# Optimization experiments

Hardware: AMD Instinct MI355X
Metric: run time of the kernel (lower is better)

Reference implementation:

```python
import jax, jax.numpy as jnp
import numpy as np

EMBED, HEADS, LEVELS, POINTS = 256, 8, 4, 4
SPATIAL_SHAPES = np.array([[128, 128], [64, 64], [32, 32], [16, 16]], dtype=np.int32)


def _grid_init_bias():
    # Faithful reproduction of the sampling_offsets bias init (per-head directional grid).
    thetas = np.arange(HEADS, dtype=np.float32) * (2.0 * np.pi / HEADS)
    g = np.stack([np.cos(thetas), np.sin(thetas)], -1)
    g = g / np.abs(g).max(-1, keepdims=True)
    g = np.tile(g.reshape(HEADS, 1, 1, 2), (1, LEVELS, POINTS, 1))
    for i in range(POINTS):
        g[:, :, i, :] *= i + 1
    return g.reshape(-1).astype(np.float32)


def setup_inputs() -> dict:
    key = jax.random.key(0)
    ks = jax.random.split(key, 8)
    bs = 2
    V = int((SPATIAL_SHAPES[:, 0] * SPATIAL_SHAPES[:, 1]).sum())  # 21760
    Q = V  # encoder self-attention
    C = EMBED
    n_off = HEADS * LEVELS * POINTS * 2
    n_attn = HEADS * LEVELS * POINTS
    inv_sqrt_c = 1.0 / np.sqrt(C)
    return {
        "query": jax.random.normal(ks[0], (bs, Q, C), jnp.float32),
        "value": jax.random.normal(ks[1], (bs, V, C), jnp.float32),
        "reference_points": jax.random.uniform(ks[2], (bs, Q, LEVELS, 2), jnp.float32),
        "spatial_shapes": SPATIAL_SHAPES,  # static int array
        # learned parameters (torch Linear stored as [in, out]: y = x @ W + b)
        "W_off": jax.random.normal(ks[3], (C, n_off), jnp.float32) * 0.01,
        "b_off": jnp.asarray(_grid_init_bias()),
        "W_attn": jax.random.normal(ks[4], (C, n_attn), jnp.float32) * 0.02,
        "b_attn": jnp.zeros((n_attn,), jnp.float32),
        "W_v": jax.random.normal(ks[5], (C, C), jnp.float32) * inv_sqrt_c,
        "b_v": jnp.zeros((C,), jnp.float32),
        "W_out": jax.random.normal(ks[6], (C, C), jnp.float32) * inv_sqrt_c,
        "b_out": jnp.zeros((C,), jnp.float32),
    }


def _ms_deform_attn(query, value, reference_points, shapes,
                    W_off, b_off, W_attn, b_attn, W_v, b_v, W_out, b_out):
    bs, Q, C = query.shape
    d = C // HEADS
    # value projection -> [bs, heads, V, d]
    val = (value @ W_v + b_v).reshape(bs, -1, HEADS, d).transpose(0, 2, 1, 3)
    # sampling offsets and attention weights from query
    off = (query @ W_off + b_off).reshape(bs, Q, HEADS, LEVELS, POINTS, 2)
    attn = jax.nn.softmax(
        (query @ W_attn + b_attn).reshape(bs, Q, HEADS, LEVELS * POINTS), axis=-1
    ).reshape(bs, Q, HEADS, LEVELS, POINTS)
    # offset normalizer is (W, H) per level
    norm = jnp.asarray(np.stack([shapes[:, 1], shapes[:, 0]], -1), jnp.float32)  # [L,2]
    loc = reference_points[:, :, None, :, None, :] + off / norm[None, None, None, :, None, :]

    out = jnp.zeros((bs, HEADS, Q, d), query.dtype)
    start = 0
    for l in range(LEVELS):
        H, W = int(shapes[l, 0]), int(shapes[l, 1])
        v_l = val[:, :, start:start + H * W]  # [bs, heads, H*W, d]
        start += H * W
        loc_l = loc[:, :, :, l]    # [bs, Q, heads, P, 2] in [0,1]
        attn_l = attn[:, :, :, l]  # [bs, Q, heads, P]
        # grid_sample(align_corners=False, padding_mode='zeros') semantics
        g = 2.0 * loc_l - 1.0
        x = (g[..., 0] + 1.0) * 0.5 * W - 0.5
        y = (g[..., 1] + 1.0) * 0.5 * H - 0.5
        x0 = jnp.floor(x)
        y0 = jnp.floor(y)
        for dx in (0, 1):
            for dy in (0, 1):
                xi = x0 + dx
                yi = y0 + dy
                w = (1.0 - jnp.abs(x - xi)) * (1.0 - jnp.abs(y - yi))
                valid = (xi >= 0) & (xi <= W - 1) & (yi >= 0) & (yi <= H - 1)
                w = jnp.where(valid, w, 0.0) * attn_l  # fused corner + attention weight
                idx = (jnp.clip(yi, 0, H - 1).astype(jnp.int32) * W
                       + jnp.clip(xi, 0, W - 1).astype(jnp.int32))  # [bs,Q,heads,P]
                idx_t = jnp.transpose(idx, (0, 2, 1, 3)).reshape(bs, HEADS, Q * POINTS)
                vals = jnp.take_along_axis(v_l, idx_t[..., None], axis=2)
                vals = vals.reshape(bs, HEADS, Q, POINTS, d)
                out = out + jnp.einsum('bhqpd,bqhp->bhqd', vals, w)
    out = out.transpose(0, 2, 1, 3).reshape(bs, Q, C)  # heads-major channel layout
    return out @ W_out + b_out


def reference(query, value, reference_points, spatial_shapes,
              W_off, b_off, W_attn, b_attn, W_v, b_v, W_out, b_out):
    shapes = np.asarray(spatial_shapes)  # static
    return _ms_deform_attn(query, value, reference_points, shapes,
                           W_off, b_off, W_attn, b_attn, W_v, b_v, W_out, b_out)
```

## Files before the change

kernel.cpp:

```cpp
#include <hip/hip_runtime.h>
#include <math.h>

#define QN 21760
#define MTOT 43520
#define SZBQC 11141120

typedef __attribute__((ext_vector_type(8))) short bf16x8;
typedef __attribute__((ext_vector_type(4))) float f32x4;

__device__ inline ushort f2bf(float f) {
  union { float f; uint u; } v; v.f = f;
  return (ushort)((v.u + 0x7FFFu + ((v.u >> 16) & 1u)) >> 16);
}
__device__ inline uint pk2(float lo, float hi) { return (uint)f2bf(lo) | ((uint)f2bf(hi) << 16); }

__device__ inline void g2l(const ushort* g, ushort* l) {
  __builtin_amdgcn_global_load_lds(
      (const __attribute__((address_space(1))) void*)g,
      (__attribute__((address_space(3))) void*)l, 16, 0, 0);
}

__global__ __launch_bounds__(256) void prep_weights(
    const float* __restrict__ Wv, const float* __restrict__ Wout,
    const float* __restrict__ Woff, const float* __restrict__ Wattn,
    const float* __restrict__ boff, const float* __restrict__ battn,
    ushort* __restrict__ wv_t, ushort* __restrict__ wout_t,
    ushort* __restrict__ wol_t, float* __restrict__ biasf) {
  int bidx = blockIdx.x, t = threadIdx.x;
  if (bidx < 256) {
    int idx = bidx * 256 + t; int n = idx >> 8, k = idx & 255;
    wv_t[idx] = f2bf(Wv[(size_t)k * 256 + n]);
  } else if (bidx < 512) {
    int idx = (bidx - 256) * 256 + t; int n = idx >> 8, k = idx & 255;
    wout_t[idx] = f2bf(Wout[(size_t)k * 256 + n]);
  } else {
    int idx = (bidx - 512) * 256 + t; int n = idx >> 8, k = idx & 255;
    float v = (n < 256) ? Woff[(size_t)k * 256 + n] : Wattn[(size_t)k * 128 + (n - 256)];
    wol_t[idx] = f2bf(v);
    if (idx < 384) biasf[idx] = (idx < 256) ? boff[idx] : battn[idx - 256];
  }
}


__global__ __launch_bounds__(256) void gemm_in(
    const float* __restrict__ value, const float* __restrict__ query,
    const ushort* __restrict__ Wv, const ushort* __restrict__ Wol,
    const float* __restrict__ bv, const float* __restrict__ bol,
    ushort* __restrict__ val_out, float* __restrict__ offlog) {
  __shared__ ushort As[2][4096];
  __shared__ ushort Bs[2][4096];
  const int bid = blockIdx.x;
  const int q5  = bid >> 3;
  const int bxv = (bid & 7) + 8 * (q5 / 5);
  const int bx  = q5 % 5;
  if (bxv >= 340) return;
  const int t = threadIdx.x, wave = t >> 6, lane = t & 63;
  const int bm = bxv * 128;
  const bool isVal = bx < 2;
  const float* A   = isVal ? value : query;
  const ushort* Bt = isVal ? (Wv + (size_t)bx * 128 * 256)
                           : (Wol + (size_t)(bx - 2) * 128 * 256);
  const int wm = (wave >> 1) * 64, wn = (wave & 1) * 64;
  const int l15 = lane & 15, l4 = lane >> 4;
  const int pc = l4 ^ ((l15 >> 1) & 3);

  const int srow = lane >> 2;
  const int sch  = (lane & 3) ^ ((lane >> 3) & 3);
  const ushort* Bg = Bt + (size_t)(32 * wave + srow) * 256 + sch * 8;
  ushort* lb[2] = { &Bs[0][(32 * wave) * 32], &Bs[1][(32 * wave) * 32] };

  f32x4 acc[4][4];
#pragma unroll
  for (int i = 0; i < 4; ++i)
#pragma unroll
    for (int j = 0; j < 4; ++j) acc[i][j] = (f32x4){0.f, 0.f, 0.f, 0.f};

  int arow[4], apart[4];
#pragma unroll
  for (int i = 0; i < 4; ++i) {
    int c = t + i * 256; arow[i] = c >> 3; apart[i] = c & 7;
  }

  {
    float4 pa[4];
#pragma unroll
    for (int i = 0; i < 4; ++i)
      pa[i] = *(const float4*)&A[(size_t)(bm + arow[i]) * 256 + apart[i] * 4];
    g2l(Bg, lb[0]); g2l(Bg + 16 * 256, lb[0] + 16 * 32);
#pragma unroll
    for (int i = 0; i < 4; ++i) {
      int pc16 = (apart[i] >> 1) ^ ((arow[i] >> 1) & 3);
      ushort4 hv = { f2bf(pa[i].x), f2bf(pa[i].y), f2bf(pa[i].z), f2bf(pa[i].w) };
      *(ushort4*)&As[0][arow[i] * 32 + pc16 * 8 + (apart[i] & 1) * 4] = hv;
    }
  }

  for (int k = 0; k < 8; ++k) {
    __syncthreads();
    const int cur = k & 1, nxt = cur ^ 1;
    float4 pa[4];
    if (k < 7) {
      int k1 = (k + 1) * 32;
#pragma unroll
      for (int i = 0; i < 4; ++i)
        pa[i] = *(const float4*)&A[(size_t)(bm + arow[i]) * 256 + k1 + apart[i] * 4];
      g2l(Bg + k1, lb[nxt]); g2l(Bg + 16 * 256 + k1, lb[nxt] + 16 * 32);
    }
    bf16x8 af[4], bfr[4];
#pragma unroll
    for (int mi = 0; mi < 4; ++mi)
      af[mi] = *(const bf16x8*)&As[cur][(wm + mi * 16 + l15) * 32 + pc * 8];
#pragma unroll
    for (int ni = 0; ni < 4; ++ni)
      bfr[ni] = *(const bf16x8*)&Bs[cur][(wn + ni * 16 + l15) * 32 + pc * 8];
#pragma unroll
    for (int mi = 0; mi < 4; ++mi)
#pragma unroll
      for (int ni = 0; ni < 4; ++ni)
        acc[mi][ni] = __builtin_amdgcn_mfma_f32_16x16x32_bf16(af[mi], bfr[ni], acc[mi][ni], 0, 0, 0);
    if (k < 7) {
#pragma unroll
      for (int i = 0; i < 4; ++i) {
        int pc16 = (apart[i] >> 1) ^ ((arow[i] >> 1) & 3);
        ushort4 hv = { f2bf(pa[i].x), f2bf(pa[i].y), f2bf(pa[i].z), f2bf(pa[i].w) };
        *(ushort4*)&As[nxt][arow[i] * 32 + pc16 * 8 + (apart[i] & 1) * 4] = hv;
      }
    }
  }

  if (isVal) {
    _Float16* vo = (_Float16*)val_out;
#pragma unroll
    for (int mi = 0; mi < 4; ++mi)
#pragma unroll
      for (int ni = 0; ni < 4; ++ni) {
        int col = bx * 128 + wn + ni * 16 + l15;
        float bb = bv[col];
        int hh = col >> 5, c = col & 31;
#pragma unroll
        for (int r = 0; r < 4; ++r) {
          int row = bm + wm + mi * 16 + l4 * 4 + r;
          int b = (row >= QN) ? 1 : 0;
          int vpos = row - b * QN;
          vo[((size_t)(b * 8 + hh) * QN + vpos) * 32 + c] = (_Float16)(acc[mi][ni][r] + bb);
        }
      }
  } else {
#pragma unroll
    for (int mi = 0; mi < 4; ++mi)
#pragma unroll
      for (int ni = 0; ni < 4; ++ni) {
        int col = (bx - 2) * 128 + wn + ni * 16 + l15;
        float bb = bol[col];
#pragma unroll
        for (int r = 0; r < 4; ++r) {
          int row = bm + wm + mi * 16 + l4 * 4 + r;
          offlog[(size_t)row * 384 + col] = acc[mi][ni][r] + bb;
        }
      }
  }
}

__global__ __launch_bounds__(256) void gemm_out(
    const ushort* __restrict__ A, const ushort* __restrict__ Bt,
    const float* __restrict__ bias, float* __restrict__ C) {
  __shared__ ushort As[2][4096];
  __shared__ ushort Bs[2][4096];
  const int bid = blockIdx.x;
  const int q2  = bid >> 3;
  const int bxv = (bid & 7) + 8 * (q2 >> 1);
  const int byv = q2 & 1;
  if (bxv >= 340) return;
  const int t = threadIdx.x, wave = t >> 6, lane = t & 63;
  const int bm = bxv * 128, bn = byv * 128;
  const int wm = (wave >> 1) * 64, wn = (wave & 1) * 64;
  const int l15 = lane & 15, l4 = lane >> 4;
  const int pc = l4 ^ ((l15 >> 1) & 3);

  const int srow = lane >> 2;
  const int sch  = (lane & 3) ^ ((lane >> 3) & 3);
  const ushort* Ag = A + (size_t)(bm + 32 * wave + srow) * 256 + sch * 8;
  const ushort* Bg = Bt + (size_t)(bn + 32 * wave + srow) * 256 + sch * 8;
  ushort* la[2] = { &As[0][(32 * wave) * 32], &As[1][(32 * wave) * 32] };
  ushort* lb[2] = { &Bs[0][(32 * wave) * 32], &Bs[1][(32 * wave) * 32] };

  f32x4 acc[4][4];
#pragma unroll
  for (int i = 0; i < 4; ++i)
#pragma unroll
    for (int j = 0; j < 4; ++j) acc[i][j] = (f32x4){0.f, 0.f, 0.f, 0.f};

  g2l(Ag, la[0]); g2l(Ag + 16 * 256, la[0] + 16 * 32);
  g2l(Bg, lb[0]); g2l(Bg + 16 * 256, lb[0] + 16 * 32);

  for (int k = 0; k < 8; ++k) {
    __syncthreads();
    const int cur = k & 1, nxt = cur ^ 1;
    if (k < 7) {
      int k1 = (k + 1) * 32;
      g2l(Ag + k1, la[nxt]); g2l(Ag + 16 * 256 + k1, la[nxt] + 16 * 32);
      g2l(Bg + k1, lb[nxt]); g2l(Bg + 16 * 256 + k1, lb[nxt] + 16 * 32);
    }
    bf16x8 af[4], bfr[4];
#pragma unroll
    for (int mi = 0; mi < 4; ++mi)
      af[mi] = *(const bf16x8*)&As[cur][(wm + mi * 16 + l15) * 32 + pc * 8];
#pragma unroll
    for (int ni = 0; ni < 4; ++ni)
      bfr[ni] = *(const bf16x8*)&Bs[cur][(wn + ni * 16 + l15) * 32 + pc * 8];
#pragma unroll
    for (int mi = 0; mi < 4; ++mi)
#pragma unroll
      for (int ni = 0; ni < 4; ++ni)
        acc[mi][ni] = __builtin_amdgcn_mfma_f32_16x16x32_bf16(af[mi], bfr[ni], acc[mi][ni], 0, 0, 0);
  }

#pragma unroll
  for (int mi = 0; mi < 4; ++mi)
#pragma unroll
    for (int ni = 0; ni < 4; ++ni) {
      int col = bn + wn + ni * 16 + l15;
      float bb = bias[col];
#pragma unroll
      for (int r = 0; r < 4; ++r) {
        int row = bm + wm + mi * 16 + l4 * 4 + r;
        C[(size_t)row * 256 + col] = acc[mi][ni][r] + bb;
      }
    }
}

__device__ inline void fmah(float* a, uint4 u, float wv) {
  union { uint4 u; _Float16 h[8]; } c; c.u = u;
#pragma unroll
  for (int i = 0; i < 8; ++i) a[i] = fmaf((float)c.h[i], wv, a[i]);
}

__global__ __launch_bounds__(256) void msda_sample(
    const ushort* __restrict__ val, const float* __restrict__ offlog,
    const float* __restrict__ ref, ushort* __restrict__ interm) {
  int h   = blockIdx.x & 7;
  int z   = blockIdx.x >> 3;
  int sub = threadIdx.x & 3;
  int bq  = z * 64 + (threadIdx.x >> 2);
  int b   = (bq >= QN) ? 1 : 0;
  const uint sub8 = (uint)(sub * 8);
  const ushort* vb = val + (size_t)((uint)(b * 8 + h) * (uint)QN) * 32u + sub8;

  const float* lgp = offlog + (size_t)bq * 384 + 256 + h * 16;
  float4 lg = *(const float4*)(lgp + sub * 4);
  float m = fmaxf(fmaxf(lg.x, lg.y), fmaxf(lg.z, lg.w));
  m = fmaxf(m, __shfl_xor(m, 1, 64));
  m = fmaxf(m, __shfl_xor(m, 2, 64));
  float e0 = __expf(lg.x - m), e1 = __expf(lg.y - m),
        e2 = __expf(lg.z - m), e3 = __expf(lg.w - m);
  float s = e0 + e1 + e2 + e3;
  s += __shfl_xor(s, 1, 64);
  s += __shfl_xor(s, 2, 64);
  float inv = __builtin_amdgcn_rcpf(s);
  float aw[4] = { e0 * inv, e1 * inv, e2 * inv, e3 * inv };

  const int  Wl  = 128 >> sub;
  const uint t16 = 65536u >> (sub + sub);
  const int  lst = (int)((65536u - t16) / 3u);
  const float fW = (float)Wl;
  const float* offp = offlog + (size_t)bq * 384 + h * 32;
  float4 o0 = *(const float4*)(offp + sub * 8);
  float4 o1 = *(const float4*)(offp + sub * 8 + 4);
  float2 rf = *(const float2*)(ref + (size_t)bq * 8 + sub * 2);
  const float xb = rf.x * fW - 0.5f;
  const float yb = rf.y * fW - 0.5f;
  float ox[4] = { o0.x, o0.z, o1.x, o1.z };
  float oy[4] = { o0.y, o0.w, o1.y, o1.w };

  uint  pA0[4], pA1[4], pDX[4];
  float pX0[4], pX1[4], pY0[4], pY1[4];
#pragma unroll
  for (int p = 0; p < 4; ++p) {
    float x = xb + ox[p], y = yb + oy[p];
    float x0f = floorf(x), y0f = floorf(y);
    float fx = x - x0f, fy = y - y0f;
    int x0 = (int)x0f, y0 = (int)y0f;
    float a = aw[p];
    pX0[p] = ((uint)x0       < (uint)Wl) ? (1.f - fx) : 0.f;
    pX1[p] = ((uint)(x0 + 1) < (uint)Wl) ? fx         : 0.f;
    pY0[p] = (((uint)y0       < (uint)Wl) ? (1.f - fy) : 0.f) * a;
    pY1[p] = (((uint)(y0 + 1) < (uint)Wl) ? fy         : 0.f) * a;
    int xc0 = min(max(x0, 0), Wl - 1);
    int xc1 = min(max(x0 + 1, 0), Wl - 1);
    int yc0 = min(max(y0, 0), Wl - 1);
    int yc1 = min(max(y0 + 1, 0), Wl - 1);
    pA0[p] = (uint)((lst + yc0 * Wl + xc0) * 32);
    pA1[p] = (uint)((lst + yc1 * Wl + xc0) * 32);
    pDX[p] = (uint)((xc1 - xc0) * 32);
  }

  float acc[8];
#pragma unroll
  for (int i = 0; i < 8; ++i) acc[i] = 0.f;

  const int lanebase = (threadIdx.x & 63) & 60;
#pragma unroll
  for (int l = 0; l < 4; ++l) {
    const int src = lanebase | l;
#pragma unroll
    for (int p = 0; p < 4; ++p) {
      uint  A0  = (uint)__shfl((int)pA0[p], src, 64);
      uint  A1  = (uint)__shfl((int)pA1[p], src, 64);
      uint  DX  = (uint)__shfl((int)pDX[p], src, 64);
      float wx0 = __shfl(pX0[p], src, 64);
      float wx1 = __shfl(pX1[p], src, 64);
      float wy0 = __shfl(pY0[p], src, 64);
      float wy1 = __shfl(pY1[p], src, 64);
      uint4 u00 = *(const uint4*)(vb + A0);
      uint4 u01 = *(const uint4*)(vb + A0 + DX);
      uint4 u10 = *(const uint4*)(vb + A1);
      uint4 u11 = *(const uint4*)(vb + A1 + DX);
      fmah(acc, u00, wx0 * wy0);
      fmah(acc, u01, wx1 * wy0);
      fmah(acc, u10, wx0 * wy1);
      fmah(acc, u11, wx1 * wy1);
    }
  }

  uint4 o;
  o.x = pk2(acc[0], acc[1]); o.y = pk2(acc[2], acc[3]);
  o.z = pk2(acc[4], acc[5]); o.w = pk2(acc[6], acc[7]);
  *(uint4*)(interm + (size_t)bq * 256 + h * 32 + sub * 8) = o;
}

extern "C" void kernel_launch(void* const* d_in, const int* in_sizes, int n_in,
                              void* d_out, int out_size, void* d_ws, size_t ws_size,
                              hipStream_t stream) {
  const float* query = (const float*)d_in[0];
  const float* value = (const float*)d_in[1];
  const float* ref   = (const float*)d_in[2];
  const float* W_off  = (const float*)d_in[4];
  const float* b_off  = (const float*)d_in[5];
  const float* W_attn = (const float*)d_in[6];
  const float* b_attn = (const float*)d_in[7];
  const float* W_v    = (const float*)d_in[8];
  const float* b_v    = (const float*)d_in[9];
  const float* W_out  = (const float*)d_in[10];
  const float* b_out  = (const float*)d_in[11];
  float* out = (float*)d_out;

  char* wsb = (char*)d_ws;
  ushort* ws_wv     = (ushort*)(wsb + 0);
  ushort* ws_wol    = (ushort*)(wsb + 131072);
  ushort* ws_wout   = (ushort*)(wsb + 327680);
  float*  ws_biasf  = (float*)(wsb + 458752);
  ushort* ws_val    = (ushort*)(wsb + 462848);
  ushort* ws_interm = (ushort*)(wsb + 22745088);
  float*  ws_offlog = (float*)(wsb + 45027328);
  size_t need = (size_t)45027328 + 66846720;
  if (ws_size < need) return;

  dim3 blk(256);
  prep_weights<<<dim3(896), blk, 0, stream>>>(W_v, W_out, W_off, W_attn, b_off, b_attn,
                                              ws_wv, ws_wout, ws_wol, ws_biasf);
  gemm_in<<<dim3(1720), blk, 0, stream>>>(value, query, ws_wv, ws_wol, b_v, ws_biasf,
                                          ws_val, ws_offlog);
  msda_sample<<<dim3(5440), blk, 0, stream>>>(ws_val, ws_offlog, ref, ws_interm);
  gemm_out<<<dim3(688), blk, 0, stream>>>(ws_interm, ws_wout, b_out, out);
}
```

Before: 277.3 us.

## Pre-cast GEMM inputs to bf16, software-pipeline sampling gathers, use 2D grids

A new path converts value and query to bf16 in a prep pass whenever the workspace is large enough. The input GEMM can then stream bf16 tiles straight into LDS with direct global-to-LDS loads, replacing the in-kernel fp32 cast. The sampling kernel double-buffers its shuffle broadcasts and corner gathers, so the loads for the next point are issued before the current one is accumulated. The swizzled 1D block mapping in the GEMMs is also replaced by plain 2D grids, which may cost L2 locality and adds an extra read and write pass over the inputs.

```diff
diff --git a/kernel.cpp b/kernel.cpp
--- a/kernel.cpp
+++ b/kernel.cpp
@@ -24,8 +24,10 @@
     const float* __restrict__ Wv, const float* __restrict__ Wout,
     const float* __restrict__ Woff, const float* __restrict__ Wattn,
     const float* __restrict__ boff, const float* __restrict__ battn,
+    const float* __restrict__ value, const float* __restrict__ query,
     ushort* __restrict__ wv_t, ushort* __restrict__ wout_t,
-    ushort* __restrict__ wol_t, float* __restrict__ biasf) {
+    ushort* __restrict__ wol_t, float* __restrict__ biasf,
+    ushort* __restrict__ abf) {
   int bidx = blockIdx.x, t = threadIdx.x;
   if (bidx < 256) {
     int idx = bidx * 256 + t; int n = idx >> 8, k = idx & 255;
@@ -33,29 +35,121 @@
   } else if (bidx < 512) {
     int idx = (bidx - 256) * 256 + t; int n = idx >> 8, k = idx & 255;
     wout_t[idx] = f2bf(Wout[(size_t)k * 256 + n]);
-  } else {
+  } else if (bidx < 896) {
     int idx = (bidx - 512) * 256 + t; int n = idx >> 8, k = idx & 255;
     float v = (n < 256) ? Woff[(size_t)k * 256 + n] : Wattn[(size_t)k * 128 + (n - 256)];
     wol_t[idx] = f2bf(v);
     if (idx < 384) biasf[idx] = (idx < 256) ? boff[idx] : battn[idx - 256];
-  }
-}
-
-
-__global__ __launch_bounds__(256) void gemm_in(
+  } else {
+    int idx = (bidx - 896) * 2048 + t * 8;
+    const float* s = (idx < SZBQC) ? (value + idx) : (query + (idx - SZBQC));
+    float4 a = *(const float4*)s;
+    float4 c = *(const float4*)(s + 4);
+    uint4 o;
+    o.x = pk2(a.x, a.y); o.y = pk2(a.z, a.w);
+    o.z = pk2(c.x, c.y); o.w = pk2(c.z, c.w);
+    *(uint4*)&abf[idx] = o;
+  }
+}
+
+
+__global__ __launch_bounds__(256) void gemm_in_g2l(
+    const ushort* __restrict__ abf,
+    const ushort* __restrict__ Wv, const ushort* __restrict__ Wol,
+    const float* __restrict__ bv, const float* __restrict__ bol,
+    ushort* __restrict__ val_out, float* __restrict__ offlog) {
+  __shared__ ushort As[2][4096];
+  __shared__ ushort Bs[2][4096];
+  const int t = threadIdx.x, wave = t >> 6, lane = t & 63;
+  const int bx = blockIdx.y, bm = blockIdx.x * 128;
+  const bool isVal = bx < 2;
+  const ushort* A  = abf + (isVal ? 0 : SZBQC);
+  const ushort* Bt = isVal ? (Wv + (size_t)bx * 128 * 256)
+                           : (Wol + (size_t)(bx - 2) * 128 * 256);
+  const int wm = (wave >> 1) * 64, wn = (wave & 1) * 64;
+  const int l15 = lane & 15, l4 = lane >> 4;
+  const int pc = l4 ^ ((l15 >> 1) & 3);
+
+  const int srow = lane >> 2;
+  const int sch  = (lane & 3) ^ ((lane >> 3) & 3);
+  const ushort* Ag = A + (size_t)(bm + 32 * wave + srow) * 256 + sch * 8;
+  const ushort* Bg = Bt + (size_t)(32 * wave + srow) * 256 + sch * 8;
+  ushort* la[2] = { &As[0][(32 * wave) * 32], &As[1][(32 * wave) * 32] };
+  ushort* lb[2] = { &Bs[0][(32 * wave) * 32], &Bs[1][(32 * wave) * 32] };
+
+  f32x4 acc[4][4];
+#pragma unroll
+  for (int i = 0; i < 4; ++i)
+#pragma unroll
+    for (int j = 0; j < 4; ++j) acc[i][j] = (f32x4){0.f, 0.f, 0.f, 0.f};
+
+  g2l(Ag, la[0]); g2l(Ag + 16 * 256, la[0] + 16 * 32);
+  g2l(Bg, lb[0]); g2l(Bg + 16 * 256, lb[0] + 16 * 32);
+
+  for (int k = 0; k < 8; ++k) {
+    __syncthreads();
+    const int cur = k & 1, nxt = cur ^ 1;
+    if (k < 7) {
+      int k1 = (k + 1) * 32;
+      g2l(Ag + k1, la[nxt]); g2l(Ag + 16 * 256 + k1, la[nxt] + 16 * 32);
+      g2l(Bg + k1, lb[nxt]); g2l(Bg + 16 * 256 + k1, lb[nxt] + 16 * 32);
+    }
+    bf16x8 af[4], bfr[4];
+#pragma unroll
+    for (int mi = 0; mi < 4; ++mi)
+      af[mi] = *(const bf16x8*)&As[cur][(wm + mi * 16 + l15) * 32 + pc * 8];
+#pragma unroll
+    for (int ni = 0; ni < 4; ++ni)
+      bfr[ni] = *(const bf16x8*)&Bs[cur][(wn + ni * 16 + l15) * 32 + pc * 8];
+#pragma unroll
+    for (int mi = 0; mi < 4; ++mi)
+#pragma unroll
+      for (int ni = 0; ni < 4; ++ni)
+        acc[mi][ni] = __builtin_amdgcn_mfma_f32_16x16x32_bf16(af[mi], bfr[ni], acc[mi][ni], 0, 0, 0);
+  }
+
+  if (isVal) {
+    _Float16* vo = (_Float16*)val_out;
+#pragma unroll
+    for (int mi = 0; mi < 4; ++mi)
+#pragma unroll
+      for (int ni = 0; ni < 4; ++ni) {
+        int col = bx * 128 + wn + ni * 16 + l15;
+        float bb = bv[col];
+        int hh = col >> 5, c = col & 31;
+#pragma unroll
+        for (int r = 0; r < 4; ++r) {
+          int row = bm + wm + mi * 16 + l4 * 4 + r;
+          int b = (row >= QN) ? 1 : 0;
+          int vpos = row - b * QN;
+          vo[((size_t)(b * 8 + hh) * QN + vpos) * 32 + c] = (_Float16)(acc[mi][ni][r] + bb);
+        }
+      }
+  } else {
+#pragma unroll
+    for (int mi = 0; mi < 4; ++mi)
+#pragma unroll
+      for (int ni = 0; ni < 4; ++ni) {
+        int col = (bx - 2) * 128 + wn + ni * 16 + l15;
+        float bb = bol[col];
+#pragma unroll
+        for (int r = 0; r < 4; ++r) {
+          int row = bm + wm + mi * 16 + l4 * 4 + r;
+          offlog[(size_t)row * 384 + col] = acc[mi][ni][r] + bb;
+        }
+      }
+  }
+}
+
+__global__ __launch_bounds__(256) void gemm_in_cast(
     const float* __restrict__ value, const float* __restrict__ query,
     const ushort* __restrict__ Wv, const ushort* __restrict__ Wol,
     const float* __restrict__ bv, const float* __restrict__ bol,
     ushort* __restrict__ val_out, float* __restrict__ offlog) {
   __shared__ ushort As[2][4096];
   __shared__ ushort Bs[2][4096];
-  const int bid = blockIdx.x;
-  const int q5  = bid >> 3;
-  const int bxv = (bid & 7) + 8 * (q5 / 5);
-  const int bx  = q5 % 5;
-  if (bxv >= 340) return;
   const int t = threadIdx.x, wave = t >> 6, lane = t & 63;
-  const int bm = bxv * 128;
+  const int bx = blockIdx.y, bm = blockIdx.x * 128;
   const bool isVal = bx < 2;
   const float* A   = isVal ? value : query;
   const ushort* Bt = isVal ? (Wv + (size_t)bx * 128 * 256)
@@ -166,13 +260,8 @@
     const float* __restrict__ bias, float* __restrict__ C) {
   __shared__ ushort As[2][4096];
   __shared__ ushort Bs[2][4096];
-  const int bid = blockIdx.x;
-  const int q2  = bid >> 3;
-  const int bxv = (bid & 7) + 8 * (q2 >> 1);
-  const int byv = q2 & 1;
-  if (bxv >= 340) return;
   const int t = threadIdx.x, wave = t >> 6, lane = t & 63;
-  const int bm = bxv * 128, bn = byv * 128;
+  const int bm = blockIdx.x * 128, bn = blockIdx.y * 128;
   const int wm = (wave >> 1) * 64, wn = (wave & 1) * 64;
   const int l15 = lane & 15, l4 = lane >> 4;
   const int pc = l4 ^ ((l15 >> 1) & 3);
@@ -299,28 +388,42 @@
   for (int i = 0; i < 8; ++i) acc[i] = 0.f;
 
   const int lanebase = (threadIdx.x & 63) & 60;
-#pragma unroll
-  for (int l = 0; l < 4; ++l) {
-    const int src = lanebase | l;
-#pragma unroll
-    for (int p = 0; p < 4; ++p) {
-      uint  A0  = (uint)__shfl((int)pA0[p], src, 64);
-      uint  A1  = (uint)__shfl((int)pA1[p], src, 64);
-      uint  DX  = (uint)__shfl((int)pDX[p], src, 64);
-      float wx0 = __shfl(pX0[p], src, 64);
-      float wx1 = __shfl(pX1[p], src, 64);
-      float wy0 = __shfl(pY0[p], src, 64);
-      float wy1 = __shfl(pY1[p], src, 64);
-      uint4 u00 = *(const uint4*)(vb + A0);
-      uint4 u01 = *(const uint4*)(vb + A0 + DX);
-      uint4 u10 = *(const uint4*)(vb + A1);
-      uint4 u11 = *(const uint4*)(vb + A1 + DX);
-      fmah(acc, u00, wx0 * wy0);
-      fmah(acc, u01, wx1 * wy0);
-      fmah(acc, u10, wx0 * wy1);
-      fmah(acc, u11, wx1 * wy1);
-    }
-  }
+
+  uint  bA0[2], bA1[2], bDX[2];
+  float bX0[2], bX1[2], bY0[2], bY1[2];
+  uint4 u00[2], u01[2], u10[2], u11[2];
+
+#define MSDA_BCAST(J, S) do {                                   \
+    const int l_ = (J) >> 2, p_ = (J) & 3;                      \
+    const int src_ = lanebase | l_;                             \
+    bA0[S] = (uint)__shfl((int)pA0[p_], src_, 64);              \
+    bA1[S] = (uint)__shfl((int)pA1[p_], src_, 64);              \
+    bDX[S] = (uint)__shfl((int)pDX[p_], src_, 64);              \
+    bX0[S] = __shfl(pX0[p_], src_, 64);                         \
+    bX1[S] = __shfl(pX1[p_], src_, 64);                         \
+    bY0[S] = __shfl(pY0[p_], src_, 64);                         \
+    bY1[S] = __shfl(pY1[p_], src_, 64);                         \
+  } while (0)
+#define MSDA_LOAD(S) do {                                       \
+    u00[S] = *(const uint4*)(vb + bA0[S]);                      \
+    u01[S] = *(const uint4*)(vb + bA0[S] + bDX[S]);             \
+    u10[S] = *(const uint4*)(vb + bA1[S]);                      \
+    u11[S] = *(const uint4*)(vb + bA1[S] + bDX[S]);             \
+  } while (0)
+
+  MSDA_BCAST(0, 0);
+  MSDA_LOAD(0);
+#pragma unroll
+  for (int j = 0; j < 16; ++j) {
+    const int cur = j & 1, nxt = cur ^ 1;
+    if (j < 15) { MSDA_BCAST(j + 1, nxt); MSDA_LOAD(nxt); }
+    fmah(acc, u00[cur], bX0[cur] * bY0[cur]);
+    fmah(acc, u01[cur], bX1[cur] * bY0[cur]);
+    fmah(acc, u10[cur], bX0[cur] * bY1[cur]);
+    fmah(acc, u11[cur], bX1[cur] * bY1[cur]);
+  }
+#undef MSDA_BCAST
+#undef MSDA_LOAD
 
   uint4 o;
   o.x = pk2(acc[0], acc[1]); o.y = pk2(acc[2], acc[3]);
@@ -352,14 +455,23 @@
   ushort* ws_val    = (ushort*)(wsb + 462848);
   ushort* ws_interm = (ushort*)(wsb + 22745088);
   float*  ws_offlog = (float*)(wsb + 45027328);
-  size_t need = (size_t)45027328 + 66846720;
-  if (ws_size < need) return;
+  ushort* ws_abf    = (ushort*)(wsb + 111874048);
+  size_t need_base = (size_t)45027328 + 66846720;
+  size_t need_big  = need_base + 44564480;
+  if (ws_size < need_base) return;
+  const bool big = (ws_size >= need_big);
 
   dim3 blk(256);
-  prep_weights<<<dim3(896), blk, 0, stream>>>(W_v, W_out, W_off, W_attn, b_off, b_attn,
-                                              ws_wv, ws_wout, ws_wol, ws_biasf);
-  gemm_in<<<dim3(1720), blk, 0, stream>>>(value, query, ws_wv, ws_wol, b_v, ws_biasf,
-                                          ws_val, ws_offlog);
+  prep_weights<<<dim3(big ? 11776 : 896), blk, 0, stream>>>(
+      W_v, W_out, W_off, W_attn, b_off, b_attn, value, query,
+      ws_wv, ws_wout, ws_wol, ws_biasf, ws_abf);
+  if (big) {
+    gemm_in_g2l<<<dim3(340, 5), blk, 0, stream>>>(ws_abf, ws_wv, ws_wol, b_v, ws_biasf,
+                                                  ws_val, ws_offlog);
+  } else {
+    gemm_in_cast<<<dim3(340, 5), blk, 0, stream>>>(value, query, ws_wv, ws_wol, b_v, ws_biasf,
+                                                   ws_val, ws_offlog);
+  }
   msda_sample<<<dim3(5440), blk, 0, stream>>>(ws_val, ws_offlog, ref, ws_interm);
-  gemm_out<<<dim3(688), blk, 0, stream>>>(ws_interm, ws_wout, b_out, out);
-}
+  gemm_out<<<dim3(340, 2), blk, 0, stream>>>(ws_interm, ws_wout, b_out, out);
+}
```

New measurement: 279.4 us. About the same (+0.8%).
